# Performance work log

Hardware: AMD Instinct MI355X
Metric: run time of the kernel (lower is better)

## Reference

```python
import jax, jax.numpy as jnp
import numpy as np

B, P, T = 64, 49, 20      # batch, num_pixels (7x7), caption length
V, E, D, A, ENC = 32000, 512, 512, 512, 2048


def setup_inputs() -> dict:
    key = jax.random.key(0)
    ks = jax.random.split(key, 20)
    s = 0.02
    return {
        "features": jax.random.normal(ks[0], (B, P, ENC), jnp.float32),
        "captions": jax.random.randint(ks[1], (B, T), 0, V, jnp.int64),
        "embed_table": jax.random.normal(ks[2], (V, E), jnp.float32) * s,
        "W_ih": jax.random.normal(ks[3], (4 * D, ENC + E), jnp.float32) * s,
        "b_ih": jnp.zeros((4 * D,), jnp.float32),
        "W_hh": jax.random.normal(ks[4], (4 * D, D), jnp.float32) * s,
        "b_hh": jnp.zeros((4 * D,), jnp.float32),
        "W_init_h": jax.random.normal(ks[5], (ENC, D), jnp.float32) * s,
        "b_init_h": jnp.zeros((D,), jnp.float32),
        "W_init_c": jax.random.normal(ks[6], (ENC, D), jnp.float32) * s,
        "b_init_c": jnp.zeros((D,), jnp.float32),
        "W_enc_att": jax.random.normal(ks[7], (ENC, A), jnp.float32) * s,
        "b_enc_att": jnp.zeros((A,), jnp.float32),
        "W_dec_att": jax.random.normal(ks[8], (D, A), jnp.float32) * s,
        "b_dec_att": jnp.zeros((A,), jnp.float32),
        "w_A": jax.random.normal(ks[9], (A,), jnp.float32) * s,
        "b_A": jnp.zeros((), jnp.float32),
        "W_out": jax.random.normal(ks[10], (D, V), jnp.float32) * s,
        "b_out": jnp.zeros((V,), jnp.float32),
    }


def reference(features, captions, embed_table, W_ih, b_ih, W_hh, b_hh,
              W_init_h, b_init_h, W_init_c, b_init_c,
              W_enc_att, b_enc_att, W_dec_att, b_dec_att, w_A, b_A,
              W_out, b_out):
    # Dropout is treated as identity (eval mode) for a deterministic baseline.
    bsz, seq_len = captions.shape
    emb = embed_table[captions]                              # [B,T,E]
    mean_f = features.mean(axis=1)                           # [B,ENC]
    h0 = mean_f @ W_init_h + b_init_h                        # [B,D]
    c0 = mean_f @ W_init_c + b_init_c                        # [B,D]
    enc_states = features @ W_enc_att + b_enc_att            # [B,P,A] (precomputed, loop-invariant)

    def step(carry, x_t):
        h, c = carry
        dec = h @ W_dec_att + b_dec_att                      # [B,A]
        comb = jnp.tanh(enc_states + dec[:, None, :])        # [B,P,A]
        scores = comb @ w_A + b_A                            # [B,P]
        alpha = jax.nn.softmax(scores, axis=1)
        ctx = jnp.einsum('bpe,bp->be', features, alpha)      # [B,ENC]
        x = jnp.concatenate([ctx, x_t], axis=1)              # [B,ENC+E]
        gates = x @ W_ih.T + b_ih + h @ W_hh.T + b_hh        # [B,4D]
        i, f, g, o = jnp.split(gates, 4, axis=1)
        i, f, o = jax.nn.sigmoid(i), jax.nn.sigmoid(f), jax.nn.sigmoid(o)
        g = jnp.tanh(g)
        c2 = f * c + i * g
        h2 = o * jnp.tanh(c2)
        logits = h2 @ W_out + b_out                          # [B,V]
        return (h2, c2), logits

    xs = jnp.swapaxes(emb[:, :seq_len - 1], 0, 1)            # [T-1,B,E]
    _, preds = jax.lax.scan(step, (h0, c0), xs)              # [T-1,B,V]
    preds = jnp.swapaxes(preds, 0, 1)                        # [B,T-1,V]
    vocab = W_out.shape[1]
    last = jnp.zeros((bsz, 1, vocab), preds.dtype)           # t = T-1 never written
    return jnp.concatenate([preds, last], axis=1)            # [B,T,V]
```

## Files before the change

### kernel.cpp

```cpp
#include <hip/hip_runtime.h>

constexpr int B_   = 64;
constexpr int P_   = 49;
constexpr int T_   = 20;
constexpr int V_   = 32000;
constexpr int E_   = 512;
constexpr int D_   = 512;
constexpr int A_   = 512;
constexpr int ENC_ = 2048;
constexpr int NT_  = T_ - 1;
constexpr int KX_  = ENC_ + E_ + D_;
constexpr int KSPL = 8;
constexpr int GCH  = (KX_ / 64) / KSPL;

#define DI __device__ __forceinline__

using u16 = unsigned short;
typedef short   bf16x8 __attribute__((ext_vector_type(8)));
typedef float   f32x4  __attribute__((ext_vector_type(4)));
typedef u16     u16x4  __attribute__((ext_vector_type(4)));

DI float sigm(float x) { return 1.0f / (1.0f + __expf(-x)); }
DI float tanhx(float x) {
  x = fminf(15.0f, fmaxf(-15.0f, x));
  float e = __expf(2.0f * x);
  return (e - 1.0f) / (e + 1.0f);
}
DI u16 f2bf(float x) {
  union { float f; unsigned u; } v{x};
  unsigned r = v.u + 0x7FFF + ((v.u >> 16) & 1);
  return (u16)(r >> 16);
}
DI float bf2f(u16 x) {
  union { unsigned u; float f; } v;
  v.u = ((unsigned)x) << 16;
  return v.f;
}
DI f32x4 mfma16(bf16x8 a, bf16x8 b, f32x4 c) {
  return __builtin_amdgcn_mfma_f32_16x16x32_bf16(a, b, c, 0, 0, 0);
}


__global__ __launch_bounds__(256) void k_mean_bf(const float* __restrict__ feat,
                                                 u16* __restrict__ mfb) {
  int idx = blockIdx.x * 256 + threadIdx.x;
  int b = idx >> 11, e = idx & (ENC_ - 1);
  const float* f = feat + (size_t)b * P_ * ENC_ + e;
  float s = 0.f;
#pragma unroll
  for (int p = 0; p < P_; p++) s += f[(size_t)p * ENC_];
  mfb[idx] = f2bf(s * (1.0f / P_));
}

__global__ __launch_bounds__(256) void k_tr_cvt(const float* __restrict__ in,
    u16* __restrict__ outp, int R, int C) {
  __shared__ float tbuf[32][33];
  int tx = threadIdx.x & 31, ty = threadIdx.x >> 5;
  int c0 = blockIdx.x * 32, r0 = blockIdx.y * 32;
#pragma unroll
  for (int i = 0; i < 4; i++)
    tbuf[ty + 8 * i][tx] = in[(size_t)(r0 + ty + 8 * i) * C + c0 + tx];
  __syncthreads();
#pragma unroll
  for (int i = 0; i < 4; i++)
    outp[(size_t)(c0 + ty + 8 * i) * R + r0 + tx] = f2bf(tbuf[tx][ty + 8 * i]);
}

__global__ __launch_bounds__(256) void k_cvt4(const float* __restrict__ in,
                                              u16* __restrict__ o) {
  int i = blockIdx.x * 256 + threadIdx.x;
  float4 v = ((const float4*)in)[i];
  u16x4 r = {f2bf(v.x), f2bf(v.y), f2bf(v.z), f2bf(v.w)};
  ((u16x4*)o)[i] = r;
}

__global__ __launch_bounds__(256) void k_wg4(const float* __restrict__ Wih,
    const float* __restrict__ Whh, u16* __restrict__ Wg) {
  int i = blockIdx.x * 256 + threadIdx.x;
  int j = i / 768, rem = i - j * 768;
  int k = rem * 4;
  const float* src = (k < ENC_ + E_) ? (Wih + (size_t)j * (ENC_ + E_) + k)
                                     : (Whh + (size_t)j * D_ + (k - ENC_ - E_));
  float4 v = *(const float4*)src;
  u16x4 r = {f2bf(v.x), f2bf(v.y), f2bf(v.z), f2bf(v.w)};
  ((u16x4*)Wg)[i] = r;
}

__global__ __launch_bounds__(256) void k_emb_bf(const int* __restrict__ cap,
    const float* __restrict__ tab, u16* __restrict__ embb) {
  int idx = blockIdx.x * 256 + threadIdx.x;
  int e = idx & (E_ - 1);
  int tb = idx >> 9;
  int b = tb & 63, t = tb >> 6;
  embb[idx] = f2bf(tab[(size_t)cap[b * T_ + t] * E_ + e]);
}

__global__ __launch_bounds__(256) void k_init_bf(const u16* __restrict__ mfb,
    const u16* __restrict__ WiT, const float* __restrict__ binh,
    const float* __restrict__ binc, u16* __restrict__ hbf, float* __restrict__ c) {
  int wid = threadIdx.x >> 6, lane = threadIdx.x & 63;
  int n0 = blockIdx.x * 64 + wid * 16;
  int l16 = lane & 15, lk = lane >> 4;
  const u16* bp = WiT + (size_t)(n0 + l16) * ENC_ + 8 * lk;
  const u16* ap = mfb + (size_t)l16 * ENC_ + 8 * lk;
  f32x4 acc[4] = {};
#pragma unroll 4
  for (int kc = 0; kc < ENC_; kc += 32) {
    bf16x8 b = *(const bf16x8*)(bp + kc);
#pragma unroll
    for (int mf = 0; mf < 4; mf++) {
      bf16x8 a = *(const bf16x8*)(ap + (size_t)mf * 16 * ENC_ + kc);
      acc[mf] = mfma16(a, b, acc[mf]);
    }
  }
  int n = n0 + l16;
#pragma unroll
  for (int mf = 0; mf < 4; mf++) {
    int m = mf * 16 + 4 * lk;
#pragma unroll
    for (int r = 0; r < 4; r++) {
      float v = acc[mf][r];
      if (n < D_) hbf[(size_t)(m + r) * D_ + n] = f2bf(v + binh[n]);
      else        c[(size_t)(m + r) * D_ + (n - D_)] = v + binc[n - D_];
    }
  }
}


__global__ __launch_bounds__(256) void k_enc_bf(const u16* __restrict__ fb,
    const u16* __restrict__ WeT, const float* __restrict__ benc,
    float* __restrict__ encs) {
  int wid = threadIdx.x >> 6, lane = threadIdx.x & 63;
  int m0 = blockIdx.x * 64, n0 = blockIdx.y * 64 + wid * 16;
  int l16 = lane & 15, lk = lane >> 4;
  const u16* ap = fb + (size_t)(m0 + l16) * ENC_ + 8 * lk;
  const u16* bp = WeT + (size_t)(n0 + l16) * ENC_ + 8 * lk;
  f32x4 acc[4] = {};
#pragma unroll 8
  for (int i = 0; i < ENC_ / 32; i++) {
    int kc = i * 32;
    bf16x8 b = *(const bf16x8*)(bp + kc);
#pragma unroll
    for (int mf = 0; mf < 4; mf++) {
      bf16x8 a = *(const bf16x8*)(ap + (size_t)mf * 16 * ENC_ + kc);
      acc[mf] = mfma16(a, b, acc[mf]);
    }
  }
  float bv = benc[n0 + l16];
#pragma unroll
  for (int mf = 0; mf < 4; mf++) {
    int m = m0 + mf * 16 + 4 * lk;
#pragma unroll
    for (int r = 0; r < 4; r++)
      encs[(size_t)(m + r) * A_ + n0 + l16] = acc[mf][r] + bv;
  }
}

__global__ __launch_bounds__(256) void k_gates_bf(const u16* __restrict__ ctxb,
    const u16* __restrict__ embb, const u16* __restrict__ hbf,
    const u16* __restrict__ Wg, float* __restrict__ gp, int t) {
  int wid = threadIdx.x >> 6, lane = threadIdx.x & 63;
  int j0 = blockIdx.x * 64 + wid * 16;
  int sp = blockIdx.y;
  int l16 = lane & 15, lk = lane >> 4;
  const u16* bp = Wg + (size_t)(j0 + l16) * KX_ + 8 * lk;
  f32x4 acc[4] = {};
#pragma unroll
  for (int i = 0; i < KX_ / KSPL / 32; i++) {
    int kc = sp * (KX_ / KSPL) + i * 32;
    int k = kc + 8 * lk;
    bf16x8 b = *(const bf16x8*)(bp + kc);
#pragma unroll
    for (int mf = 0; mf < 4; mf++) {
      int row = mf * 16 + l16;
      const u16* src;
      if (k < ENC_)            src = ctxb + (size_t)row * ENC_ + k;
      else if (k < ENC_ + E_)  src = embb + ((size_t)t * B_ + row) * E_ + (k - ENC_);
      else                     src = hbf + (size_t)row * D_ + (k - ENC_ - E_);
      bf16x8 a = *(const bf16x8*)src;
      acc[mf] = mfma16(a, b, acc[mf]);
    }
  }
#pragma unroll
  for (int mf = 0; mf < 4; mf++) {
    int m = mf * 16 + 4 * lk;
#pragma unroll
    for (int r = 0; r < 4; r++)
      gp[((size_t)sp * B_ + m + r) * (4 * D_) + j0 + l16] = acc[mf][r];
  }
}

__global__ __launch_bounds__(256) void k_logits_all2(const u16* __restrict__ hall,
    const u16* __restrict__ WoT, const float* __restrict__ bout,
    float* __restrict__ out) {
  int wid = threadIdx.x >> 6, lane = threadIdx.x & 63;
  int n0 = blockIdx.x * 64 + wid * 16;
  int l16 = lane & 15, lk = lane >> 4;
  bf16x8 bfr[16];
  const u16* bp = WoT + (size_t)(n0 + l16) * D_ + 8 * lk;
#pragma unroll
  for (int kc = 0; kc < 16; kc++) bfr[kc] = *(const bf16x8*)(bp + kc * 32);
  float bv = bout[n0 + l16];
#pragma unroll 1
  for (int s = 0; s < NT_; s++) {
    const u16* ap = hall + (size_t)s * B_ * D_ + (size_t)l16 * D_ + 8 * lk;
    f32x4 acc[4] = {};
#pragma unroll
    for (int kc = 0; kc < 16; kc++) {
#pragma unroll
      for (int mf = 0; mf < 4; mf++) {
        bf16x8 a = *(const bf16x8*)(ap + (size_t)mf * 16 * D_ + kc * 32);
        acc[mf] = mfma16(a, bfr[kc], acc[mf]);
      }
    }
#pragma unroll
    for (int mf = 0; mf < 4; mf++) {
      int m = mf * 16 + 4 * lk;
#pragma unroll
      for (int r = 0; r < 4; r++)
        out[((size_t)(m + r) * T_ + s) * V_ + n0 + l16] = acc[mf][r] + bv;
    }
  }
#pragma unroll
  for (int mf = 0; mf < 4; mf++) {
    int m = mf * 16 + 4 * lk;
#pragma unroll
    for (int r = 0; r < 4; r++)
      out[((size_t)(m + r) * T_ + (T_ - 1)) * V_ + n0 + l16] = 0.f;
  }
}


__global__ __launch_bounds__(512) void k_att3(const u16* __restrict__ featb,
    const float* __restrict__ encs, const u16* __restrict__ WdT,
    const float* __restrict__ bdec, const float* __restrict__ wA,
    const float* __restrict__ bA, const float* __restrict__ gp,
    const float* __restrict__ bih, const float* __restrict__ bhh,
    const float* __restrict__ c_in, float* __restrict__ c_out,
    u16* __restrict__ hbf, u16* __restrict__ hallp, u16* __restrict__ ctxb,
    int do_reduce, int do_att) {
  __shared__ u16 hsb[D_];
  __shared__ float ds[A_];
  __shared__ float sc[P_];
  __shared__ float inv_s;
  int b = blockIdx.x, y = blockIdx.y, tid = threadIdx.x;

  if (do_reduce) {
    int d = tid;
    float g0 = 0, g1 = 0, g2 = 0, g3 = 0;
#pragma unroll
    for (int s = 0; s < KSPL; s++) {
      const float* g = gp + (size_t)(s * B_ + b) * (4 * D_);
      g0 += g[d]; g1 += g[D_ + d]; g2 += g[2 * D_ + d]; g3 += g[3 * D_ + d];
    }
    g0 += bih[d] + bhh[d];
    g1 += bih[D_ + d] + bhh[D_ + d];
    g2 += bih[2 * D_ + d] + bhh[2 * D_ + d];
    g3 += bih[3 * D_ + d] + bhh[3 * D_ + d];
    float iv = sigm(g0), fv = sigm(g1), gv = tanhx(g2), ov = sigm(g3);
    float cv = fmaf(fv, c_in[b * D_ + d], iv * gv);
    float hv = ov * tanhx(cv);
    u16 hb = f2bf(hv);
    hsb[d] = hb;
    if (y == 0) {
      c_out[b * D_ + d] = cv;
      hbf[b * D_ + d] = hb;
      hallp[b * D_ + d] = hb;
    }
  } else {
    hsb[tid] = hbf[b * D_ + tid];
  }
  __syncthreads();
  if (!do_att) return;

  {
    int w = tid >> 6, lane = tid & 63, l16 = lane & 15, lk = lane >> 4;
#pragma unroll
    for (int f = 0; f < 4; f++) {
      int n = w * 64 + f * 16 + l16;
      const u16* bp = WdT + (size_t)n * D_ + 8 * lk;
      f32x4 acc = {};
#pragma unroll
      for (int kc = 0; kc < D_; kc += 32) {
        bf16x8 av = *(const bf16x8*)(hsb + kc + 8 * lk);
        bf16x8 bv = *(const bf16x8*)(bp + kc);
        acc = mfma16(av, bv, acc);
      }
      if (lk == 0) ds[n] = acc[0] + bdec[n];
    }
  }
  __syncthreads();

  int wv_ = tid >> 6, ln = tid & 63;
  float bA0 = bA[0];
  for (int p = wv_; p < P_; p += 8) {
    const float* ep = encs + (size_t)(b * P_ + p) * A_;
    float s = 0.f;
#pragma unroll
    for (int a = ln; a < A_; a += 64) s += tanhx(ep[a] + ds[a]) * wA[a];
#pragma unroll
    for (int off = 32; off; off >>= 1) s += __shfl_down(s, off);
    if (ln == 0) sc[p] = s + bA0;
  }
  __syncthreads();

  if (tid == 0) {
    float mx = -1e30f;
    for (int p = 0; p < P_; p++) mx = fmaxf(mx, sc[p]);
    float sum = 0.f;
    for (int p = 0; p < P_; p++) { float ex = __expf(sc[p] - mx); sc[p] = ex; sum += ex; }
    inv_s = 1.0f / sum;
  }
  __syncthreads();

  float inv = inv_s;
#pragma unroll
  for (int q = 0; q < 2; q++) {
    int e = y * 1024 + q * 512 + tid;
    const u16* fp = featb + (size_t)b * P_ * ENC_ + e;
    float s = 0.f;
#pragma unroll
    for (int p = 0; p < P_; p++) s = fmaf(bf2f(fp[(size_t)p * ENC_]), sc[p], s);
    ctxb[b * ENC_ + e] = f2bf(s * inv);
  }
}


DI int swz(int row, int slot) { return row * 64 + ((slot ^ (row >> 2)) << 2); }

__global__ __launch_bounds__(256) void k_mean(const float* __restrict__ feat,
                                              float* __restrict__ mf) {
  int idx = blockIdx.x * 256 + threadIdx.x;
  int b = idx >> 11, e = idx & (ENC_ - 1);
  const float* f = feat + (size_t)b * P_ * ENC_ + e;
  float s = 0.f;
#pragma unroll
  for (int p = 0; p < P_; p++) s += f[(size_t)p * ENC_];
  mf[idx] = s * (1.0f / P_);
}

__global__ __launch_bounds__(256) void k_emb(const int* __restrict__ cap,
                                             const float* __restrict__ tab,
                                             float* __restrict__ emb) {
  int idx = blockIdx.x * 256 + threadIdx.x;
  int e  = idx & (E_ - 1);
  int bt = idx >> 9;
  int b = bt / NT_, t = bt - b * NT_;
  int tok = cap[b * T_ + t];
  emb[idx] = tab[(size_t)tok * E_ + e];
}

__global__ __launch_bounds__(256) void k_init(const float* __restrict__ mf,
    const float* __restrict__ Wh, const float* __restrict__ bh,
    const float* __restrict__ Wc, const float* __restrict__ bc,
    float* __restrict__ h, float* __restrict__ c) {
  __shared__ float ms[ENC_];
  int b = blockIdx.y;
  for (int i = threadIdx.x; i < ENC_; i += 256) ms[i] = mf[b * ENC_ + i];
  __syncthreads();
  int d = blockIdx.x * 256 + threadIdx.x;
  const float* W = blockIdx.z ? Wc : Wh;
  float s = (blockIdx.z ? bc : bh)[d];
#pragma unroll 8
  for (int e = 0; e < ENC_; e++) s = fmaf(ms[e], W[(size_t)e * D_ + d], s);
  (blockIdx.z ? c : h)[b * D_ + d] = s;
}

__global__ __launch_bounds__(256) void k_zero_last(float* __restrict__ out) {
  int i = blockIdx.x * 256 + threadIdx.x;
  int b = i / 8000, v4 = i - b * 8000;
  float4 z = {0.f, 0.f, 0.f, 0.f};
  *(float4*)(out + ((size_t)b * T_ + (T_ - 1)) * V_ + (size_t)v4 * 4) = z;
}

__global__ __launch_bounds__(256) void k_enc(const float* __restrict__ Ag,
    const float* __restrict__ Wg, const float* __restrict__ bias,
    float* __restrict__ Cg) {
  __shared__ float As[64 * 64], Ws[64 * 64];
  int m0 = blockIdx.x * 64, n0 = blockIdx.y * 64;
  int tid = threadIdx.x, tn = tid & 15, tm = tid >> 4;
  float acc[4][4] = {};
#pragma unroll 1
  for (int ch = 0; ch < ENC_ / 64; ch++) {
    int k0 = ch * 64;
    __syncthreads();
#pragma unroll
    for (int q = 0; q < 4; q++) {
      int idx = tid + q * 256;
      int row = idx >> 4, slot = idx & 15;
      *(float4*)&As[swz(row, slot)] =
          *(const float4*)(Ag + (size_t)(m0 + row) * ENC_ + k0 + slot * 4);
      *(float4*)&Ws[swz(row, slot)] =
          *(const float4*)(Wg + (size_t)(k0 + row) * A_ + n0 + slot * 4);
    }
    __syncthreads();
#pragma unroll
    for (int kk = 0; kk < 16; kk++) {
      float4 av[4], wv[4];
#pragma unroll
      for (int i = 0; i < 4; i++) av[i] = *(float4*)&As[swz(4 * tm + i, kk)];
#pragma unroll
      for (int u = 0; u < 4; u++) wv[u] = *(float4*)&Ws[swz(4 * kk + u, tn)];
      const float* wq = (const float*)wv;
#pragma unroll
      for (int i = 0; i < 4; i++) {
        const float* aq = (const float*)&av[i];
#pragma unroll
        for (int j = 0; j < 4; j++) {
          float s = acc[i][j];
#pragma unroll
          for (int u = 0; u < 4; u++) s = fmaf(aq[u], wq[u * 4 + j], s);
          acc[i][j] = s;
        }
      }
    }
  }
#pragma unroll
  for (int i = 0; i < 4; i++) {
    int m = m0 + 4 * tm + i, n = n0 + 4 * tn;
    float4 bv = *(const float4*)(bias + n);
    float4 o = {acc[i][0] + bv.x, acc[i][1] + bv.y, acc[i][2] + bv.z, acc[i][3] + bv.w};
    *(float4*)(Cg + (size_t)m * A_ + n) = o;
  }
}

__global__ __launch_bounds__(256) void k_logits(const float* __restrict__ h,
    const float* __restrict__ Wout, const float* __restrict__ bout,
    float* __restrict__ out, int t) {
  __shared__ float As[64 * 64], Ws[64 * 64];
  int n0 = blockIdx.x * 64;
  int tid = threadIdx.x, tn = tid & 15, tm = tid >> 4;
  float acc[4][4] = {};
#pragma unroll 1
  for (int ch = 0; ch < D_ / 64; ch++) {
    int k0 = ch * 64;
    __syncthreads();
#pragma unroll
    for (int q = 0; q < 4; q++) {
      int idx = tid + q * 256;
      int row = idx >> 4, slot = idx & 15;
      *(float4*)&As[swz(row, slot)] =
          *(const float4*)(h + (size_t)row * D_ + k0 + slot * 4);
      *(float4*)&Ws[swz(row, slot)] =
          *(const float4*)(Wout + (size_t)(k0 + row) * V_ + n0 + slot * 4);
    }
    __syncthreads();
#pragma unroll
    for (int kk = 0; kk < 16; kk++) {
      float4 av[4], wv[4];
#pragma unroll
      for (int i = 0; i < 4; i++) av[i] = *(float4*)&As[swz(4 * tm + i, kk)];
#pragma unroll
      for (int u = 0; u < 4; u++) wv[u] = *(float4*)&Ws[swz(4 * kk + u, tn)];
      const float* wq = (const float*)wv;
#pragma unroll
      for (int i = 0; i < 4; i++) {
        const float* aq = (const float*)&av[i];
#pragma unroll
        for (int j = 0; j < 4; j++) {
          float s = acc[i][j];
#pragma unroll
          for (int u = 0; u < 4; u++) s = fmaf(aq[u], wq[u * 4 + j], s);
          acc[i][j] = s;
        }
      }
    }
  }
#pragma unroll
  for (int i = 0; i < 4; i++) {
    int m = 4 * tm + i, n = n0 + 4 * tn;
    float4 bv = *(const float4*)(bout + n);
    float4 o = {acc[i][0] + bv.x, acc[i][1] + bv.y, acc[i][2] + bv.z, acc[i][3] + bv.w};
    *(float4*)(out + ((size_t)m * T_ + t) * V_ + n) = o;
  }
}

__global__ __launch_bounds__(256) void k_gates(const float* __restrict__ ctx,
    const float* __restrict__ emb, const float* __restrict__ h,
    const float* __restrict__ Wih, const float* __restrict__ Whh,
    float* __restrict__ gp, int t) {
  __shared__ float As[64 * 64], Ws[64 * 64];
  int n0 = blockIdx.x * 64;
  int sp = blockIdx.y;
  int tid = threadIdx.x, tn = tid & 15, tm = tid >> 4;
  float acc[4][4] = {};
#pragma unroll 1
  for (int ch = 0; ch < GCH; ch++) {
    int k0 = sp * (GCH * 64) + ch * 64;
    __syncthreads();
#pragma unroll
    for (int q = 0; q < 4; q++) {
      int idx = tid + q * 256;
      int row = idx >> 4, slot = idx & 15;
      int k = k0 + slot * 4;
      float4 xv;
      if (k < ENC_)            xv = *(const float4*)(ctx + (size_t)row * ENC_ + k);
      else if (k < ENC_ + E_)  xv = *(const float4*)(emb + ((size_t)row * NT_ + t) * E_ + (k - ENC_));
      else                     xv = *(const float4*)(h + (size_t)row * D_ + (k - ENC_ - E_));
      *(float4*)&As[swz(row, slot)] = xv;
      int j = n0 + row;
      float4 wv2;
      if (k < ENC_ + E_) wv2 = *(const float4*)(Wih + (size_t)j * (ENC_ + E_) + k);
      else               wv2 = *(const float4*)(Whh + (size_t)j * D_ + (k - ENC_ - E_));
      *(float4*)&Ws[swz(row, slot)] = wv2;
    }
    __syncthreads();
#pragma unroll
    for (int kk = 0; kk < 16; kk++) {
      float4 av[4], wv[4];
#pragma unroll
      for (int i = 0; i < 4; i++) av[i] = *(float4*)&As[swz(4 * tm + i, kk)];
#pragma unroll
      for (int j = 0; j < 4; j++) wv[j] = *(float4*)&Ws[swz(4 * tn + j, kk)];
#pragma unroll
      for (int i = 0; i < 4; i++) {
        const float* aq = (const float*)&av[i];
#pragma unroll
        for (int j = 0; j < 4; j++) {
          const float* wqj = (const float*)&wv[j];
          float s = acc[i][j];
#pragma unroll
          for (int u = 0; u < 4; u++) s = fmaf(aq[u], wqj[u], s);
          acc[i][j] = s;
        }
      }
    }
  }
#pragma unroll
  for (int i = 0; i < 4; i++) {
    int b = 4 * tm + i, j = n0 + 4 * tn;
    float4 o = {acc[i][0], acc[i][1], acc[i][2], acc[i][3]};
    *(float4*)(gp + ((size_t)(sp * B_ + b)) * (4 * D_) + j) = o;
  }
}

__global__ __launch_bounds__(512) void k_att(const float* __restrict__ feat,
    const float* __restrict__ encs, const float* __restrict__ Wdec,
    const float* __restrict__ bdec, const float* __restrict__ wA,
    const float* __restrict__ bA, const float* __restrict__ gp,
    const float* __restrict__ bih, const float* __restrict__ bhh,
    float* __restrict__ h, float* __restrict__ c, float* __restrict__ ctx,
    int do_reduce, int do_att) {
  __shared__ float hs[D_];
  __shared__ float ds[A_];
  __shared__ float sc[P_];
  __shared__ float inv_s;
  int b = blockIdx.x, tid = threadIdx.x;

  if (do_reduce) {
    int d = tid;
    float g0 = 0, g1 = 0, g2 = 0, g3 = 0;
#pragma unroll
    for (int s = 0; s < KSPL; s++) {
      const float* g = gp + (size_t)(s * B_ + b) * (4 * D_);
      g0 += g[d]; g1 += g[D_ + d]; g2 += g[2 * D_ + d]; g3 += g[3 * D_ + d];
    }
    g0 += bih[d] + bhh[d];
    g1 += bih[D_ + d] + bhh[D_ + d];
    g2 += bih[2 * D_ + d] + bhh[2 * D_ + d];
    g3 += bih[3 * D_ + d] + bhh[3 * D_ + d];
    float iv = sigm(g0), fv = sigm(g1), gv = tanhx(g2), ov = sigm(g3);
    float cv = fmaf(fv, c[b * D_ + d], iv * gv);
    float hv = ov * tanhx(cv);
    c[b * D_ + d] = cv;
    h[b * D_ + d] = hv;
    hs[d] = hv;
  } else {
    hs[tid] = h[b * D_ + tid];
  }
  __syncthreads();
  if (!do_att) return;

  {
    int a = tid;
    float s = bdec[a];
#pragma unroll 8
    for (int d = 0; d < D_; d++) s = fmaf(hs[d], Wdec[(size_t)d * A_ + a], s);
    ds[a] = s;
  }
  __syncthreads();

  int wv_ = tid >> 6, ln = tid & 63;
  float bA0 = bA[0];
  for (int p = wv_; p < P_; p += 8) {
    const float* ep = encs + (size_t)(b * P_ + p) * A_;
    float s = 0.f;
#pragma unroll
    for (int a = ln; a < A_; a += 64) s += tanhx(ep[a] + ds[a]) * wA[a];
#pragma unroll
    for (int off = 32; off; off >>= 1) s += __shfl_down(s, off);
    if (ln == 0) sc[p] = s + bA0;
  }
  __syncthreads();

  if (tid == 0) {
    float mx = -1e30f;
    for (int p = 0; p < P_; p++) mx = fmaxf(mx, sc[p]);
    float sum = 0.f;
    for (int p = 0; p < P_; p++) { float ex = __expf(sc[p] - mx); sc[p] = ex; sum += ex; }
    inv_s = 1.0f / sum;
  }
  __syncthreads();

  float inv = inv_s;
  for (int e = tid; e < ENC_; e += 512) {
    const float* fp = feat + (size_t)b * P_ * ENC_ + e;
    float s = 0.f;
#pragma unroll
    for (int p = 0; p < P_; p++) s = fmaf(fp[(size_t)p * ENC_], sc[p], s);
    ctx[b * ENC_ + e] = s * inv;
  }
}


extern "C" void kernel_launch(void* const* d_in, const int* in_sizes, int n_in,
                              void* d_out, int out_size, void* d_ws, size_t ws_size,
                              hipStream_t stream) {
  const float* features = (const float*)d_in[0];
  const int*   captions = (const int*)d_in[1];
  const float* table    = (const float*)d_in[2];
  const float* Wih  = (const float*)d_in[3];
  const float* bih  = (const float*)d_in[4];
  const float* Whh  = (const float*)d_in[5];
  const float* bhh  = (const float*)d_in[6];
  const float* Winh = (const float*)d_in[7];
  const float* binh = (const float*)d_in[8];
  const float* Winc = (const float*)d_in[9];
  const float* binc = (const float*)d_in[10];
  const float* Wenc = (const float*)d_in[11];
  const float* benc = (const float*)d_in[12];
  const float* Wdec = (const float*)d_in[13];
  const float* bdec = (const float*)d_in[14];
  const float* wA   = (const float*)d_in[15];
  const float* bA   = (const float*)d_in[16];
  const float* Wout = (const float*)d_in[17];
  const float* bout = (const float*)d_in[18];
  float* out = (float*)d_out;

  constexpr size_t F_ENC = (size_t)B_ * P_ * A_;
  constexpr size_t F_C   = (size_t)B_ * D_;
  constexpr size_t F_GP  = (size_t)KSPL * B_ * 4 * D_;
  constexpr size_t U_WOT = (size_t)V_ * D_;
  constexpr size_t U_WG  = (size_t)(4 * D_) * KX_;
  constexpr size_t U_HBF = (size_t)B_ * D_;
  constexpr size_t U_CTX = (size_t)B_ * ENC_;
  constexpr size_t U_FEAT = (size_t)B_ * P_ * ENC_;
  constexpr size_t U_WET = (size_t)A_ * ENC_;
  constexpr size_t U_EMB = (size_t)NT_ * B_ * E_;
  constexpr size_t U_WDT = (size_t)A_ * D_;
  constexpr size_t U_HALL = (size_t)NT_ * B_ * D_;
  static_assert(U_EMB + U_WDT <= U_WET, "embb+WdT overlay WeT region");
  constexpr size_t NEED_BYTES =
      (F_ENC + 2 * F_C + F_GP) * 4 +
      (U_WOT + U_WG + U_HBF + U_CTX + U_FEAT + U_WET + U_HALL) * 2;

  if (ws_size >= NEED_BYTES) {
    float* ws = (float*)d_ws;
    float* enc_states = ws;
    float* cbuf0  = enc_states + F_ENC;
    float* cbuf1  = cbuf0 + F_C;
    float* gparts = cbuf1 + F_C;
    u16* WoT   = (u16*)(gparts + F_GP);
    u16* Wg    = WoT + U_WOT;
    u16* hbf   = Wg + U_WG;
    u16* ctxb  = hbf + U_HBF;
    u16* featb = ctxb + U_CTX;
    u16* wetr  = featb + U_FEAT;
    u16* WeT   = wetr;
    u16* embb  = wetr;
    u16* WdT   = wetr + U_EMB;
    u16* hall  = wetr + U_WET;
    u16* WiT   = (u16*)gparts;
    u16* mfb   = ctxb;
    float* cb[2] = {cbuf0, cbuf1};

    k_mean_bf<<<512, 256, 0, stream>>>(features, mfb);
    k_tr_cvt<<<dim3(D_ / 32, ENC_ / 32), 256, 0, stream>>>(Winh, WiT, ENC_, D_);
    k_tr_cvt<<<dim3(D_ / 32, ENC_ / 32), 256, 0, stream>>>(Winc, WiT + (size_t)D_ * ENC_, ENC_, D_);
    k_init_bf<<<16, 256, 0, stream>>>(mfb, WiT, binh, binc, hbf, cbuf0);
    k_cvt4<<<(int)(U_FEAT / 4 / 256), 256, 0, stream>>>(features, featb);
    k_tr_cvt<<<dim3(A_ / 32, ENC_ / 32), 256, 0, stream>>>(Wenc, WeT, ENC_, A_);
    k_enc_bf<<<dim3(49, 8), 256, 0, stream>>>(featb, WeT, benc, enc_states);
    k_emb_bf<<<2432, 256, 0, stream>>>(captions, table, embb);
    k_tr_cvt<<<dim3(A_ / 32, D_ / 32), 256, 0, stream>>>(Wdec, WdT, D_, A_);
    k_tr_cvt<<<dim3(V_ / 32, D_ / 32), 256, 0, stream>>>(Wout, WoT, D_, V_);
    k_wg4<<<(int)(U_WG / 4 / 256), 256, 0, stream>>>(Wih, Whh, Wg);

    for (int t = 0; t < NT_; t++) {
      u16* hallp = (t > 0) ? (hall + (size_t)(t - 1) * B_ * D_) : hall;
      const float* cin = cb[(t > 0 ? (t - 1) : 0) & 1];
      float* cout = cb[t & 1];
      k_att3<<<dim3(64, 2), 512, 0, stream>>>(featb, enc_states, WdT, bdec, wA,
                                              bA, gparts, bih, bhh, cin, cout,
                                              hbf, hallp, ctxb, t > 0 ? 1 : 0, 1);
      k_gates_bf<<<dim3(32, KSPL), 256, 0, stream>>>(ctxb, embb, hbf, Wg, gparts, t);
    }
    k_att3<<<dim3(64, 1), 512, 0, stream>>>(featb, enc_states, WdT, bdec, wA,
                                            bA, gparts, bih, bhh,
                                            cb[(NT_ - 1) & 1], cb[NT_ & 1], hbf,
                                            hall + (size_t)(NT_ - 1) * B_ * D_,
                                            ctxb, 1, 0);
    k_logits_all2<<<500, 256, 0, stream>>>(hall, WoT, bout, out);
  } else {
    float* ws = (float*)d_ws;
    float* enc_states = ws;
    float* mean_f = enc_states + (size_t)B_ * P_ * A_;
    float* emb    = mean_f + (size_t)B_ * ENC_;
    float* h      = emb + (size_t)B_ * NT_ * E_;
    float* c      = h + (size_t)B_ * D_;
    float* ctx    = c + (size_t)B_ * D_;
    float* gparts = ctx + (size_t)B_ * ENC_;

    k_mean<<<512, 256, 0, stream>>>(features, mean_f);
    k_emb<<<2432, 256, 0, stream>>>(captions, table, emb);
    k_init<<<dim3(2, 64, 2), 256, 0, stream>>>(mean_f, Winh, binh, Winc, binc, h, c);
    k_enc<<<dim3(49, 8), 256, 0, stream>>>(features, Wenc, benc, enc_states);
    k_zero_last<<<2000, 256, 0, stream>>>(out);

    for (int t = 0; t < NT_; t++) {
      k_att<<<64, 512, 0, stream>>>(features, enc_states, Wdec, bdec, wA, bA,
                                    gparts, bih, bhh, h, c, ctx, t > 0 ? 1 : 0, 1);
      if (t > 0)
        k_logits<<<500, 256, 0, stream>>>(h, Wout, bout, out, t - 1);
      k_gates<<<dim3(32, KSPL), 256, 0, stream>>>(ctx, emb, h, Wih, Whh, gparts, t);
    }
    k_att<<<64, 512, 0, stream>>>(features, enc_states, Wdec, bdec, wA, bA,
                                  gparts, bih, bhh, h, c, ctx, 1, 0);
    k_logits<<<500, 256, 0, stream>>>(h, Wout, bout, out, NT_ - 1);
  }
}
```

Measured before the change: 1.264 ms.

## Split logits kernel across timestep groups with LDS-staged coalesced stores; vectorize ctx loads

The final logits kernel now launches four times as many blocks, each handling every fourth timestep for a 64-column vocab tile. Results are staged through shared memory so each output row is written with float4 stores instead of scattered scalar stores. The W_out fragments are reloaded per k-chunk instead of being held in registers, which lowers register pressure but adds repeated weight reads. In the attention kernel, the context reduction now loads two bf16 values per thread with a single vector load and writes them back as a pair.

```diff
diff --git a/kernel.cpp b/kernel.cpp
--- a/kernel.cpp
+++ b/kernel.cpp
@@ -19,6 +19,7 @@
 typedef short   bf16x8 __attribute__((ext_vector_type(8)));
 typedef float   f32x4  __attribute__((ext_vector_type(4)));
 typedef u16     u16x4  __attribute__((ext_vector_type(4)));
+typedef u16     u16x2  __attribute__((ext_vector_type(2)));
 
 DI float sigm(float x) { return 1.0f / (1.0f + __expf(-x)); }
 DI float tanhx(float x) {
@@ -190,43 +191,53 @@
   }
 }
 
-__global__ __launch_bounds__(256) void k_logits_all2(const u16* __restrict__ hall,
+__global__ __launch_bounds__(256) void k_logits_all3(const u16* __restrict__ hall,
     const u16* __restrict__ WoT, const float* __restrict__ bout,
     float* __restrict__ out) {
+  __shared__ float tile[64 * 68];
+  int bid = blockIdx.x;
+  int x8 = bid & 7, g = bid >> 3;
+  int sg = g & 3, ntg = g >> 2;
+  int nt = x8 + 8 * ntg;
+  if (nt >= 500) return;
   int wid = threadIdx.x >> 6, lane = threadIdx.x & 63;
-  int n0 = blockIdx.x * 64 + wid * 16;
+  int n0 = nt * 64 + wid * 16;
   int l16 = lane & 15, lk = lane >> 4;
-  bf16x8 bfr[16];
   const u16* bp = WoT + (size_t)(n0 + l16) * D_ + 8 * lk;
-#pragma unroll
-  for (int kc = 0; kc < 16; kc++) bfr[kc] = *(const bf16x8*)(bp + kc * 32);
   float bv = bout[n0 + l16];
+  int tr = threadIdx.x >> 2, tc = threadIdx.x & 3;
 #pragma unroll 1
-  for (int s = 0; s < NT_; s++) {
+  for (int s = sg; s < NT_; s += 4) {
     const u16* ap = hall + (size_t)s * B_ * D_ + (size_t)l16 * D_ + 8 * lk;
     f32x4 acc[4] = {};
 #pragma unroll
     for (int kc = 0; kc < 16; kc++) {
+      bf16x8 b = *(const bf16x8*)(bp + kc * 32);
 #pragma unroll
       for (int mf = 0; mf < 4; mf++) {
         bf16x8 a = *(const bf16x8*)(ap + (size_t)mf * 16 * D_ + kc * 32);
-        acc[mf] = mfma16(a, bfr[kc], acc[mf]);
+        acc[mf] = mfma16(a, b, acc[mf]);
       }
     }
-#pragma unroll
-    for (int mf = 0; mf < 4; mf++) {
-      int m = mf * 16 + 4 * lk;
+    __syncthreads();
+#pragma unroll
+    for (int mf = 0; mf < 4; mf++)
 #pragma unroll
       for (int r = 0; r < 4; r++)
-        out[((size_t)(m + r) * T_ + s) * V_ + n0 + l16] = acc[mf][r] + bv;
-    }
-  }
-#pragma unroll
-  for (int mf = 0; mf < 4; mf++) {
-    int m = mf * 16 + 4 * lk;
-#pragma unroll
-    for (int r = 0; r < 4; r++)
-      out[((size_t)(m + r) * T_ + (T_ - 1)) * V_ + n0 + l16] = 0.f;
+        tile[(mf * 16 + 4 * lk + r) * 68 + wid * 16 + l16] = acc[mf][r] + bv;
+    __syncthreads();
+    float* op = out + ((size_t)tr * T_ + s) * V_ + nt * 64;
+#pragma unroll
+    for (int j = 0; j < 4; j++) {
+      int cc = (tc + j * 4) * 4;
+      *(float4*)(op + cc) = *(float4*)&tile[tr * 68 + cc];
+    }
+  }
+  if (sg == 3) {
+    float4 z = {0.f, 0.f, 0.f, 0.f};
+    float* op = out + ((size_t)tr * T_ + (T_ - 1)) * V_ + nt * 64;
+#pragma unroll
+    for (int j = 0; j < 4; j++) *(float4*)(op + (tc + j * 4) * 4) = z;
   }
 }
 
@@ -313,15 +324,19 @@
   }
   __syncthreads();
 
-  float inv = inv_s;
-#pragma unroll
-  for (int q = 0; q < 2; q++) {
-    int e = y * 1024 + q * 512 + tid;
+  {
+    float inv = inv_s;
+    int e = y * 1024 + tid * 2;
     const u16* fp = featb + (size_t)b * P_ * ENC_ + e;
-    float s = 0.f;
-#pragma unroll
-    for (int p = 0; p < P_; p++) s = fmaf(bf2f(fp[(size_t)p * ENC_]), sc[p], s);
-    ctxb[b * ENC_ + e] = f2bf(s * inv);
+    float s0 = 0.f, s1 = 0.f;
+#pragma unroll
+    for (int p = 0; p < P_; p++) {
+      u16x2 w = *(const u16x2*)(fp + (size_t)p * ENC_);
+      s0 = fmaf(bf2f(w.x), sc[p], s0);
+      s1 = fmaf(bf2f(w.y), sc[p], s1);
+    }
+    u16x2 o = {f2bf(s0 * inv), f2bf(s1 * inv)};
+    *(u16x2*)(ctxb + b * ENC_ + e) = o;
   }
 }
 
@@ -700,7 +715,7 @@
                                             cb[(NT_ - 1) & 1], cb[NT_ & 1], hbf,
                                             hall + (size_t)(NT_ - 1) * B_ * D_,
                                             ctxb, 1, 0);
-    k_logits_all2<<<500, 256, 0, stream>>>(hall, WoT, bout, out);
+    k_logits_all3<<<2016, 256, 0, stream>>>(hall, WoT, bout, out);
   } else {
     float* ws = (float*)d_ws;
     float* enc_states = ws;
```

New measurement: 1.265 ms. About the same (+0.1%).
